# Kernel tuning notes

Measured on AMD Instinct MI355X. Metric: run time of the kernel, lower is better.

The kernel has to match this reference:

```python
import jax, jax.numpy as jnp
import numpy as np

E = 8        # n_experts
TOP_K = 2    # n_activated_experts
B, T, C = 4, 2048, 2048   # batch, seq, d_model
F = 5632     # expert FFN hidden (SwiGLU)


def setup_inputs() -> dict:
    key = jax.random.key(0)
    k = jax.random.split(key, 5)
    s = 0.02  # init scale keeps activations sane
    return {
        "x":  jax.random.normal(k[0], (B, T, C), jnp.float32),
        "Wg": jax.random.normal(k[1], (C, E), jnp.float32) * s,   # gate Linear (no bias)
        "W1": jax.random.normal(k[2], (E, C, F), jnp.float32) * s, # expert gate proj
        "W3": jax.random.normal(k[3], (E, C, F), jnp.float32) * s, # expert up proj
        "W2": jax.random.normal(k[4], (E, F, C), jnp.float32) * s, # expert down proj
    }


def _moe(x, Wg, W1, W3, W2, top_k=TOP_K, norm_probs=True):
    Bb, Tt, Cc = x.shape
    xf = x.reshape(-1, Cc)                                   # [N, C]
    logits = xf @ Wg                                         # [N, E]
    probs = jax.nn.softmax(logits.astype(jnp.float32), axis=-1)
    probs, indices = jax.lax.top_k(probs, top_k)             # [N, K]
    if norm_probs:
        probs = probs / probs.sum(axis=-1, keepdims=True)
    probs = probs.astype(x.dtype)
    N, Ee = xf.shape[0], W1.shape[0]
    # per-token combine weights: w[n, e] = prob if expert e selected for token n else 0
    # (top_k indices are distinct per token, so at most one add per (n, e))
    w = jnp.zeros((N, Ee), x.dtype).at[jnp.arange(N)[:, None], indices].add(probs)
    # scan over experts: weight-0 tokens contribute nothing, matching the sparse
    # masked dispatch/scatter-add of the original exactly.
    def body(y, ws):
        w1, w3, w2, we = ws                                   # we: [N]
        h = jax.nn.silu(xf @ w1) * (xf @ w3)                  # [N, F]
        return y + we[:, None] * (h @ w2), None
    y, _ = jax.lax.scan(body, jnp.zeros_like(xf), (W1, W3, W2, w.T))
    return y.reshape(Bb, Tt, Cc)


def reference(x, Wg, W1, W3, W2):
    return _moe(x, Wg, W1, W3, W2)
```

## Files before the change

### kernel.cpp

```cpp
#include <hip/hip_runtime.h>

#define N_TOK 8192
#define C_DIM 2048
#define F_DIM 5632
#define E_NUM 8
#define BK 64

#define BM 256
#define MAXT 72
#define BN1 128
#define GRID1 (MAXT * (F_DIM/BN1))
#define BN2 256
#define GRID2 (MAXT * (C_DIM/BN2))
#define NT1 (C_DIM/BK)
#define NT2 (F_DIM/BK)

typedef __attribute__((ext_vector_type(8))) short bf16x8;
typedef __attribute__((ext_vector_type(4))) float f32x4;

typedef const void __attribute__((address_space(1)))* gas1;
typedef void __attribute__((address_space(3)))* las3;

__device__ __forceinline__ unsigned short f2bf(float f){
  union { float f; unsigned u; } v; v.f = f;
  unsigned r = v.u + 0x7FFFu + ((v.u >> 16) & 1u);
  return (unsigned short)(r >> 16);
}

__device__ __forceinline__ void glds16(const unsigned short* g, unsigned short* l){
  __builtin_amdgcn_global_load_lds((gas1)g, (las3)l, 16, 0, 0);
}

#define MFMA_BF16 __builtin_amdgcn_mfma_f32_16x16x32_bf16

__global__ void k_cvt_x(const float* __restrict__ x, unsigned short* __restrict__ xb, int n4){
  int i = blockIdx.x * blockDim.x + threadIdx.x;
  int stride = gridDim.x * blockDim.x;
  const float4* xi = (const float4*)x;
  ushort4* xo = (ushort4*)xb;
  for (; i < n4; i += stride){
    float4 v = xi[i];
    ushort4 o; o.x = f2bf(v.x); o.y = f2bf(v.y); o.z = f2bf(v.z); o.w = f2bf(v.w);
    xo[i] = o;
  }
}

__global__ void k_tcvt_w(const float* __restrict__ in, unsigned short* __restrict__ out, int R, int Cc){
  __shared__ float t[64][65];
  size_t slab = (size_t)blockIdx.z * R * Cc;
  in += slab; out += slab;
  int c0 = blockIdx.x * 64, r0 = blockIdx.y * 64;
  int tx = threadIdx.x, ty = threadIdx.y;
  #pragma unroll
  for (int i = 0; i < 16; ++i){
    int r = ty + i*4;
    t[r][tx] = in[(size_t)(r0 + r) * Cc + c0 + tx];
  }
  __syncthreads();
  #pragma unroll
  for (int i = 0; i < 16; ++i){
    int cr = ty + i*4;
    out[(size_t)(c0 + cr) * R + r0 + tx] = f2bf(t[tx][cr]);
  }
}

__global__ void k_router(const float* __restrict__ x, const float* __restrict__ Wg,
                         int* __restrict__ cnt, int* __restrict__ list, float* __restrict__ p_slot)
{
  int wid = threadIdx.x >> 6, lane = threadIdx.x & 63;
  int n = blockIdx.x * 4 + wid;
  int e = lane >> 3, sub = lane & 7;
  const float* xr = x + (size_t)n * C_DIM;
  float acc = 0.f;
  for (int i0 = sub*4; i0 < C_DIM; i0 += 32){
    float4 v = *(const float4*)&xr[i0];
    acc += v.x * Wg[(i0  )*E_NUM + e];
    acc += v.y * Wg[(i0+1)*E_NUM + e];
    acc += v.z * Wg[(i0+2)*E_NUM + e];
    acc += v.w * Wg[(i0+3)*E_NUM + e];
  }
  acc += __shfl_xor(acc, 1);
  acc += __shfl_xor(acc, 2);
  acc += __shfl_xor(acc, 4);
  float lg[E_NUM];
  #pragma unroll
  for (int j = 0; j < E_NUM; ++j) lg[j] = __shfl(acc, j*8);
  if (lane == 0){
    int e1 = 0; float m1 = lg[0];
    #pragma unroll
    for (int j = 1; j < E_NUM; ++j) if (lg[j] > m1){ m1 = lg[j]; e1 = j; }
    int e2 = -1; float m2 = -1e30f;
    #pragma unroll
    for (int j = 0; j < E_NUM; ++j) if (j != e1 && lg[j] > m2){ m2 = lg[j]; e2 = j; }
    float p1 = 1.f / (1.f + __expf(m2 - m1));
    float p2 = 1.f - p1;
    int pos1 = atomicAdd(&cnt[e1], 1);
    list[e1*N_TOK + pos1] = n*2;
    p_slot[n*2] = p1;
    int pos2 = atomicAdd(&cnt[e2], 1);
    list[e2*N_TOK + pos2] = n*2 + 1;
    p_slot[n*2 + 1] = p2;
  }
}

__global__ void k_prefix(const int* __restrict__ cnt, int* __restrict__ meta){
  if (threadIdx.x == 0 && blockIdx.x == 0){
    int acc = 0, t = 0;
    for (int e = 0; e < E_NUM; ++e){
      meta[e] = acc; acc += cnt[e];
      int nt = (cnt[e] + BM - 1) / BM;
      for (int i = 0; i < nt; ++i) meta[16 + t++] = (e << 16) | i;
    }
    meta[8] = t;
  }
}

#define PHASE_ENTER() do{ __builtin_amdgcn_sched_barrier(0); __builtin_amdgcn_s_barrier(); \
                          __builtin_amdgcn_s_setprio(1); } while(0)
#define PHASE_EXIT()  do{ __builtin_amdgcn_s_setprio(0); __builtin_amdgcn_sched_barrier(0); \
                          __builtin_amdgcn_s_barrier(); } while(0)

__global__ __launch_bounds__(512, 2) void k_gemm1(
    const unsigned short* __restrict__ xb,
    const unsigned short* __restrict__ wb1,
    const unsigned short* __restrict__ wb3,
    unsigned short* __restrict__ h,
    const int* __restrict__ cnt,
    const int* __restrict__ meta,
    const int* __restrict__ list)
{
  int o = blockIdx.x;
  int w = (o & 7) * (GRID1/8) + (o >> 3);
  int t = w % MAXT;
  int n0 = (w / MAXT) * BN1;
  if (t >= meta[8]) return;
  int info = meta[16 + t];
  int e  = info >> 16;
  int m0 = (info & 0xffff) * BM;
  int count = cnt[e];
  int hbase = meta[e];

  __shared__ __align__(16) unsigned short lds[2*32768];

  int tid = threadIdx.x;
  int lane = tid & 63, wid = tid >> 6;
  int wm = wid >> 1, wn = wid & 1;
  int l15 = lane & 15;
  int xc0 = (lane >> 4) ^ (lane & 7);
  int xc1 = xc0 ^ 4;

  int srow = tid >> 3;
  int swz = ((tid & 7) ^ (srow & 7)) * 8;
  const unsigned short* aP[4];
  #pragma unroll
  for (int u = 0; u < 4; ++u){
    int ts = list[e*N_TOK + m0 + u*64 + srow];
    int tok = (ts >> 1) & (N_TOK - 1);
    aP[u] = xb + (size_t)tok * C_DIM + swz;
  }
  const unsigned short* bP[4];
  #pragma unroll
  for (int u = 0; u < 4; ++u){
    const unsigned short* base = (u < 2) ? wb1 : wb3;
    bP[u] = base + ((size_t)e*F_DIM + n0 + (u & 1)*64 + srow) * C_DIM + swz;
  }
  int ldw = wid * 512;

  #define ST_A(u, kt) glds16(aP[u] + (kt)*BK, &lds[((kt)&1)*32768 + (u)*4096 + ldw])
  #define ST_B(u, kt) glds16(bP[u] + (kt)*BK, &lds[((kt)&1)*32768 + 16384 + (u)*4096 + ldw])

  ST_A(0,0); ST_A(1,0); ST_A(2,0); ST_A(3,0);
  ST_B(0,0); ST_B(1,0); ST_B(2,0); ST_B(3,0);
  ST_A(0,1); ST_A(1,1); ST_A(2,1); ST_A(3,1);
  asm volatile("s_waitcnt vmcnt(4)" ::: "memory");
  __builtin_amdgcn_sched_barrier(0);
  __builtin_amdgcn_s_barrier();

  f32x4 zero = {0.f, 0.f, 0.f, 0.f};
  f32x4 acc1[4][4], acc3[4][4];
  #pragma unroll
  for (int m = 0; m < 4; ++m)
    #pragma unroll
    for (int q = 0; q < 4; ++q){ acc1[m][q] = zero; acc3[m][q] = zero; }

  for (int kt = 0; kt < NT1; ++kt){
    const unsigned short* bufc = &lds[(kt & 1)*32768];
    bf16x8 a[4][2], b1f[2], b3f[2];
    #pragma unroll
    for (int m = 0; m < 4; ++m){
      int row = wm*64 + m*16 + l15;
      a[m][0] = *(const bf16x8*)&bufc[row*64 + xc0*8];
      a[m][1] = *(const bf16x8*)&bufc[row*64 + xc1*8];
    }
    {
      int brow = wn*64 + l15;
      b1f[0] = *(const bf16x8*)&bufc[16384 + brow*64 + xc0*8];
      b1f[1] = *(const bf16x8*)&bufc[16384 + brow*64 + xc1*8];
      b3f[0] = *(const bf16x8*)&bufc[24576 + brow*64 + xc0*8];
      b3f[1] = *(const bf16x8*)&bufc[24576 + brow*64 + xc1*8];
    }
    ST_B(0, kt+1); ST_B(1, kt+1); ST_B(2, kt+1); ST_B(3, kt+1);
    PHASE_ENTER();
    #pragma unroll
    for (int m = 0; m < 4; ++m){
      acc1[m][0] = MFMA_BF16(a[m][0], b1f[0], acc1[m][0], 0, 0, 0);
      acc1[m][0] = MFMA_BF16(a[m][1], b1f[1], acc1[m][0], 0, 0, 0);
      acc3[m][0] = MFMA_BF16(a[m][0], b3f[0], acc3[m][0], 0, 0, 0);
      acc3[m][0] = MFMA_BF16(a[m][1], b3f[1], acc3[m][0], 0, 0, 0);
    }
    PHASE_EXIT();
    #pragma unroll
    for (int q = 1; q < 4; ++q){
      int brow = wn*64 + q*16 + l15;
      b1f[0] = *(const bf16x8*)&bufc[16384 + brow*64 + xc0*8];
      b1f[1] = *(const bf16x8*)&bufc[16384 + brow*64 + xc1*8];
      b3f[0] = *(const bf16x8*)&bufc[24576 + brow*64 + xc0*8];
      b3f[1] = *(const bf16x8*)&bufc[24576 + brow*64 + xc1*8];
      if (q == 1){ ST_A(0, kt+2); ST_A(1, kt+2); }
      if (q == 2){ ST_A(2, kt+2); ST_A(3, kt+2); }
      PHASE_ENTER();
      #pragma unroll
      for (int m = 0; m < 4; ++m){
        acc1[m][q] = MFMA_BF16(a[m][0], b1f[0], acc1[m][q], 0, 0, 0);
        acc1[m][q] = MFMA_BF16(a[m][1], b1f[1], acc1[m][q], 0, 0, 0);
        acc3[m][q] = MFMA_BF16(a[m][0], b3f[0], acc3[m][q], 0, 0, 0);
        acc3[m][q] = MFMA_BF16(a[m][1], b3f[1], acc3[m][q], 0, 0, 0);
      }
      __builtin_amdgcn_s_setprio(0);
      if (q == 3) asm volatile("s_waitcnt vmcnt(4)" ::: "memory");
      __builtin_amdgcn_sched_barrier(0);
      __builtin_amdgcn_s_barrier();
    }
  }
  asm volatile("s_waitcnt vmcnt(0)" ::: "memory");

  #pragma unroll
  for (int m = 0; m < 4; ++m){
    #pragma unroll
    for (int r = 0; r < 4; ++r){
      int rloc = m0 + wm*64 + m*16 + ((lane >> 4) * 4) + r;
      if (rloc < count){
        unsigned short* hrow = h + (size_t)(hbase + rloc) * F_DIM + n0 + wn*64 + l15;
        #pragma unroll
        for (int q = 0; q < 4; ++q){
          float v1 = acc1[m][q][r];
          float v3 = acc3[m][q][r];
          float hv = (v1 / (1.f + __expf(-v1))) * v3;
          hrow[q*16] = f2bf(hv);
        }
      }
    }
  }
  #undef ST_A
  #undef ST_B
}

__global__ __launch_bounds__(512, 2) void k_gemm2(
    const unsigned short* __restrict__ h,
    const unsigned short* __restrict__ wb2,
    float* __restrict__ y,
    const int* __restrict__ cnt,
    const int* __restrict__ meta,
    const int* __restrict__ list,
    const float* __restrict__ p_slot)
{
  int o = blockIdx.x;
  int w = (o & 7) * (GRID2/8) + (o >> 3);
  int t = w % MAXT;
  int n0 = (w / MAXT) * BN2;
  if (t >= meta[8]) return;
  int info = meta[16 + t];
  int e  = info >> 16;
  int m0 = (info & 0xffff) * BM;
  int count = cnt[e];
  int hbase = meta[e];

  __shared__ __align__(16) unsigned short lds[2*32768];

  int tid = threadIdx.x;
  int lane = tid & 63, wid = tid >> 6;
  int wm = wid >> 1, wn = wid & 1;
  int l15 = lane & 15;
  int xc0 = (lane >> 4) ^ (lane & 7);
  int xc1 = xc0 ^ 4;

  int srow = tid >> 3;
  int swz = ((tid & 7) ^ (srow & 7)) * 8;
  const unsigned short* aP[4];
  #pragma unroll
  for (int u = 0; u < 4; ++u)
    aP[u] = h + (size_t)(hbase + m0 + u*64 + srow) * F_DIM + swz;
  const unsigned short* bP[4];
  #pragma unroll
  for (int u = 0; u < 4; ++u)
    bP[u] = wb2 + ((size_t)e*C_DIM + n0 + u*64 + srow) * F_DIM + swz;
  int ldw = wid * 512;

  #define ST_A2(u, kt) glds16(aP[u] + (kt)*BK, &lds[((kt)&1)*32768 + (u)*4096 + ldw])
  #define ST_B2(u, kt) glds16(bP[u] + (kt)*BK, &lds[((kt)&1)*32768 + 16384 + (u)*4096 + ldw])

  ST_A2(0,0); ST_A2(1,0); ST_A2(2,0); ST_A2(3,0);
  ST_B2(0,0); ST_B2(1,0); ST_B2(2,0); ST_B2(3,0);
  asm volatile("s_waitcnt vmcnt(4)" ::: "memory");
  ST_A2(0,1); ST_A2(1,1); ST_A2(2,1); ST_A2(3,1);
  ST_B2(0,1); ST_B2(2,1);
  asm volatile("s_waitcnt vmcnt(6)" ::: "memory");
  __builtin_amdgcn_sched_barrier(0);
  __builtin_amdgcn_s_barrier();

  f32x4 zero = {0.f, 0.f, 0.f, 0.f};
  f32x4 acc[4][8];
  #pragma unroll
  for (int m = 0; m < 4; ++m)
    #pragma unroll
    for (int nf = 0; nf < 8; ++nf) acc[m][nf] = zero;

  for (int kt = 0; kt < NT2; ++kt){
    const unsigned short* bufc = &lds[(kt & 1)*32768];
    bf16x8 a[4][2], bf[2][2];
    #pragma unroll
    for (int m = 0; m < 4; ++m){
      int row = wm*64 + m*16 + l15;
      a[m][0] = *(const bf16x8*)&bufc[row*64 + xc0*8];
      a[m][1] = *(const bf16x8*)&bufc[row*64 + xc1*8];
    }
    #pragma unroll
    for (int j = 0; j < 2; ++j){
      int brow = wn*128 + j*16 + l15;
      bf[j][0] = *(const bf16x8*)&bufc[16384 + brow*64 + xc0*8];
      bf[j][1] = *(const bf16x8*)&bufc[16384 + brow*64 + xc1*8];
    }
    ST_B2(1, kt+1); ST_B2(3, kt+1);
    PHASE_ENTER();
    #pragma unroll
    for (int m = 0; m < 4; ++m)
      #pragma unroll
      for (int j = 0; j < 2; ++j){
        acc[m][j] = MFMA_BF16(a[m][0], bf[j][0], acc[m][j], 0, 0, 0);
        acc[m][j] = MFMA_BF16(a[m][1], bf[j][1], acc[m][j], 0, 0, 0);
      }
    PHASE_EXIT();
    #pragma unroll
    for (int q = 1; q < 4; ++q){
      #pragma unroll
      for (int j = 0; j < 2; ++j){
        int brow = wn*128 + (q*2 + j)*16 + l15;
        bf[j][0] = *(const bf16x8*)&bufc[16384 + brow*64 + xc0*8];
        bf[j][1] = *(const bf16x8*)&bufc[16384 + brow*64 + xc1*8];
      }
      if (q == 1){ ST_A2(0, kt+2); ST_A2(1, kt+2); }
      if (q == 2){ ST_A2(2, kt+2); ST_A2(3, kt+2); }
      if (q == 3){ ST_B2(0, kt+2); ST_B2(2, kt+2); }
      PHASE_ENTER();
      #pragma unroll
      for (int m = 0; m < 4; ++m)
        #pragma unroll
        for (int j = 0; j < 2; ++j){
          acc[m][q*2+j] = MFMA_BF16(a[m][0], bf[j][0], acc[m][q*2+j], 0, 0, 0);
          acc[m][q*2+j] = MFMA_BF16(a[m][1], bf[j][1], acc[m][q*2+j], 0, 0, 0);
        }
      __builtin_amdgcn_s_setprio(0);
      if (q == 3) asm volatile("s_waitcnt vmcnt(6)" ::: "memory");
      __builtin_amdgcn_sched_barrier(0);
      __builtin_amdgcn_s_barrier();
    }
  }
  asm volatile("s_waitcnt vmcnt(0)" ::: "memory");

  #pragma unroll
  for (int m = 0; m < 4; ++m){
    #pragma unroll
    for (int r = 0; r < 4; ++r){
      int rloc = m0 + wm*64 + m*16 + ((lane >> 4) * 4) + r;
      if (rloc < count){
        int ts = list[e*N_TOK + rloc];
        float p = p_slot[ts];
        int tok = ts >> 1;
        float* yr = y + (size_t)tok * C_DIM + n0 + wn*128 + l15;
        #pragma unroll
        for (int nf = 0; nf < 8; ++nf)
          atomicAdd(&yr[nf*16], p * acc[m][nf][r]);
      }
    }
  }
  #undef ST_A2
  #undef ST_B2
}

extern "C" void kernel_launch(void* const* d_in, const int* in_sizes, int n_in,
                              void* d_out, int out_size, void* d_ws, size_t ws_size,
                              hipStream_t stream)
{
  const float* x  = (const float*)d_in[0];
  const float* Wg = (const float*)d_in[1];
  const float* W1 = (const float*)d_in[2];
  const float* W3 = (const float*)d_in[3];
  const float* W2 = (const float*)d_in[4];
  float* y = (float*)d_out;
  (void)in_sizes; (void)n_in; (void)out_size; (void)ws_size;

  char* ws = (char*)d_ws;
  size_t o = 0;
  auto alloc = [&](size_t bytes)->char* {
    char* p = ws + o;
    o = (o + bytes + 255) & ~(size_t)255;
    return p;
  };
  int*    cnt    = (int*)  alloc(E_NUM * 4);
  int*    meta   = (int*)  alloc(160 * 4);
  float*  p_slot = (float*)alloc((size_t)2*N_TOK * 4);
  int*    list   = (int*)  alloc((size_t)E_NUM*N_TOK * 4);
  unsigned short* xb  = (unsigned short*)alloc((size_t)N_TOK*C_DIM * 2);
  unsigned short* wb1 = (unsigned short*)alloc((size_t)E_NUM*C_DIM*F_DIM * 2);
  unsigned short* wb3 = (unsigned short*)alloc((size_t)E_NUM*C_DIM*F_DIM * 2);
  unsigned short* wb2 = (unsigned short*)alloc((size_t)E_NUM*C_DIM*F_DIM * 2);
  unsigned short* h   = (unsigned short*)alloc((size_t)(2*N_TOK + 1024)*F_DIM * 2);

  hipMemsetAsync(cnt, 0, E_NUM * 4, stream);
  hipMemsetAsync(y, 0, (size_t)N_TOK * C_DIM * 4, stream);
  k_cvt_x<<<4096, 256, 0, stream>>>(x, xb, (N_TOK*C_DIM)/4);
  k_tcvt_w<<<dim3(F_DIM/64, C_DIM/64, E_NUM), dim3(64,4), 0, stream>>>(W1, wb1, C_DIM, F_DIM);
  k_tcvt_w<<<dim3(F_DIM/64, C_DIM/64, E_NUM), dim3(64,4), 0, stream>>>(W3, wb3, C_DIM, F_DIM);
  k_tcvt_w<<<dim3(C_DIM/64, F_DIM/64, E_NUM), dim3(64,4), 0, stream>>>(W2, wb2, F_DIM, C_DIM);
  k_router<<<N_TOK/4, 256, 0, stream>>>(x, Wg, cnt, list, p_slot);
  k_prefix<<<1, 64, 0, stream>>>(cnt, meta);
  k_gemm1<<<GRID1, 512, 0, stream>>>(xb, wb1, wb3, h, cnt, meta, list);
  k_gemm2<<<GRID2, 512, 0, stream>>>(h, wb2, y, cnt, meta, list, p_slot);
}
```

Measured before the change: 1.829 ms.

## Fuse W2 fp32-to-bf16 transpose conversion into down-projection GEMM loads

Drops the separate transpose-convert kernel for W2. The second GEMM now reads fp32 W2 directly through registers, packs it to bf16 with v_cvt_pk_bf16_f32, and writes it transposed into a swizzled LDS layout. The N tile shrinks from 256 to 128 to make room. This removes a full pass that wrote and re-read the bf16 copy of W2. In exchange each W2 tile is read in fp32 (twice the bytes) and re-read by every token tile, and each block does conversion work plus more atomic-output blocks.

```diff
diff --git a/kernel.cpp b/kernel.cpp
--- a/kernel.cpp
+++ b/kernel.cpp
@@ -10,7 +10,7 @@
 #define MAXT 72
 #define BN1 128
 #define GRID1 (MAXT * (F_DIM/BN1))
-#define BN2 256
+#define BN2 128
 #define GRID2 (MAXT * (C_DIM/BN2))
 #define NT1 (C_DIM/BK)
 #define NT2 (F_DIM/BK)
@@ -27,11 +27,18 @@
   return (unsigned short)(r >> 16);
 }
 
+__device__ __forceinline__ unsigned pkbf(float a, float b){
+  unsigned r;
+  asm("v_cvt_pk_bf16_f32 %0, %1, %2" : "=v"(r) : "v"(a), "v"(b));
+  return r;
+}
+
 __device__ __forceinline__ void glds16(const unsigned short* g, unsigned short* l){
   __builtin_amdgcn_global_load_lds((gas1)g, (las3)l, 16, 0, 0);
 }
 
 #define MFMA_BF16 __builtin_amdgcn_mfma_f32_16x16x32_bf16
+#define HSW(v) ((((v) >> 1) ^ ((v) >> 2)) & 7)
 
 __global__ void k_cvt_x(const float* __restrict__ x, unsigned short* __restrict__ xb, int n4){
   int i = blockIdx.x * blockDim.x + threadIdx.x;
@@ -257,7 +264,7 @@
 
 __global__ __launch_bounds__(512, 2) void k_gemm2(
     const unsigned short* __restrict__ h,
-    const unsigned short* __restrict__ wb2,
+    const float* __restrict__ W2,
     float* __restrict__ y,
     const int* __restrict__ cnt,
     const int* __restrict__ meta,
@@ -275,14 +282,14 @@
   int count = cnt[e];
   int hbase = meta[e];
 
-  __shared__ __align__(16) unsigned short lds[2*32768];
+  __shared__ __align__(16) unsigned short lds[2*24576];
 
   int tid = threadIdx.x;
   int lane = tid & 63, wid = tid >> 6;
   int wm = wid >> 1, wn = wid & 1;
   int l15 = lane & 15;
-  int xc0 = (lane >> 4) ^ (lane & 7);
-  int xc1 = xc0 ^ 4;
+  int xcA0 = (lane >> 4) ^ (lane & 7);
+  int xcA1 = xcA0 ^ 4;
 
   int srow = tid >> 3;
   int swz = ((tid & 7) ^ (srow & 7)) * 8;
@@ -290,47 +297,67 @@
   #pragma unroll
   for (int u = 0; u < 4; ++u)
     aP[u] = h + (size_t)(hbase + m0 + u*64 + srow) * F_DIM + swz;
-  const unsigned short* bP[4];
-  #pragma unroll
-  for (int u = 0; u < 4; ++u)
-    bP[u] = wb2 + ((size_t)e*C_DIM + n0 + u*64 + srow) * F_DIM + swz;
   int ldw = wid * 512;
-
-  #define ST_A2(u, kt) glds16(aP[u] + (kt)*BK, &lds[((kt)&1)*32768 + (u)*4096 + ldw])
-  #define ST_B2(u, kt) glds16(bP[u] + (kt)*BK, &lds[((kt)&1)*32768 + 16384 + (u)*4096 + ldw])
-
-  ST_A2(0,0); ST_A2(1,0); ST_A2(2,0); ST_A2(3,0);
-  ST_B2(0,0); ST_B2(1,0); ST_B2(2,0); ST_B2(3,0);
-  asm volatile("s_waitcnt vmcnt(4)" ::: "memory");
-  ST_A2(0,1); ST_A2(1,1); ST_A2(2,1); ST_A2(3,1);
-  ST_B2(0,1); ST_B2(2,1);
-  asm volatile("s_waitcnt vmcnt(6)" ::: "memory");
+  #define ST_A2(u, kt2) glds16(aP[u] + (kt2)*BK, &lds[((kt2)&1)*24576 + (u)*4096 + ldw])
+
+  int fT = (tid >> 5) * 4;
+  int cT = (tid & 31) * 4;
+  const float* wG = W2 + ((size_t)e * F_DIM + fT) * C_DIM + n0 + cT;
+  int fb7 = fT & 7, fb3 = fT >> 3;
+
+  #define LOADW(V, kk) do{ _Pragma("unroll") for (int r_ = 0; r_ < 4; ++r_) \
+      V[r_] = *(const float4*)(wG + (size_t)((kk)*64 + r_) * C_DIM); }while(0)
+  #define CVTW(V, pb) do{ unsigned short* bb_ = &lds[(pb)*24576 + 16384]; \
+      _Pragma("unroll") for (int i_ = 0; i_ < 4; ++i_){ \
+        int c_ = cT + i_; uint2 u_; \
+        u_.x = pkbf(((const float*)&V[0])[i_], ((const float*)&V[1])[i_]); \
+        u_.y = pkbf(((const float*)&V[2])[i_], ((const float*)&V[3])[i_]); \
+        *(uint2*)&bb_[c_*64 + ((fb3 ^ HSW(c_))*8) + fb7] = u_; } }while(0)
+
+  int bch[4], brow[4];
+  #pragma unroll
+  for (int q = 0; q < 4; ++q){
+    int cr = wn*64 + q*16 + l15;
+    bch[q] = HSW(cr); brow[q] = cr*64;
+  }
+
+  f32x4 zero = {0.f, 0.f, 0.f, 0.f};
+  f32x4 acc[4][4];
+  #pragma unroll
+  for (int m = 0; m < 4; ++m)
+    #pragma unroll
+    for (int q = 0; q < 4; ++q) acc[m][q] = zero;
+
+  float4 wv[4], wx[4];
+  LOADW(wv, 0);
+  #pragma unroll
+  for (int u = 0; u < 4; ++u) ST_A2(u, 0);
+  #pragma unroll
+  for (int u = 0; u < 4; ++u) ST_A2(u, 1);
+  CVTW(wv, 0);
+  LOADW(wv, 1);
+  asm volatile("s_waitcnt vmcnt(8)" ::: "memory");
+  asm volatile("s_waitcnt lgkmcnt(0)" ::: "memory");
   __builtin_amdgcn_sched_barrier(0);
   __builtin_amdgcn_s_barrier();
 
-  f32x4 zero = {0.f, 0.f, 0.f, 0.f};
-  f32x4 acc[4][8];
-  #pragma unroll
-  for (int m = 0; m < 4; ++m)
-    #pragma unroll
-    for (int nf = 0; nf < 8; ++nf) acc[m][nf] = zero;
-
   for (int kt = 0; kt < NT2; ++kt){
-    const unsigned short* bufc = &lds[(kt & 1)*32768];
+    const unsigned short* bufc = &lds[(kt & 1)*24576];
+    int k2 = (kt + 2 < NT2) ? kt + 2 : NT2 - 1;
     bf16x8 a[4][2], bf[2][2];
+    LOADW(wx, k2);
     #pragma unroll
     for (int m = 0; m < 4; ++m){
       int row = wm*64 + m*16 + l15;
-      a[m][0] = *(const bf16x8*)&bufc[row*64 + xc0*8];
-      a[m][1] = *(const bf16x8*)&bufc[row*64 + xc1*8];
+      a[m][0] = *(const bf16x8*)&bufc[row*64 + xcA0*8];
+      a[m][1] = *(const bf16x8*)&bufc[row*64 + xcA1*8];
     }
     #pragma unroll
     for (int j = 0; j < 2; ++j){
-      int brow = wn*128 + j*16 + l15;
-      bf[j][0] = *(const bf16x8*)&bufc[16384 + brow*64 + xc0*8];
-      bf[j][1] = *(const bf16x8*)&bufc[16384 + brow*64 + xc1*8];
-    }
-    ST_B2(1, kt+1); ST_B2(3, kt+1);
+      bf[j][0] = *(const bf16x8*)&bufc[16384 + brow[j] + (((lane>>4)    ) ^ bch[j])*8];
+      bf[j][1] = *(const bf16x8*)&bufc[16384 + brow[j] + (((lane>>4) + 4) ^ bch[j])*8];
+    }
+    CVTW(wv, (kt+1)&1);
     PHASE_ENTER();
     #pragma unroll
     for (int m = 0; m < 4; ++m)
@@ -341,29 +368,27 @@
       }
     PHASE_EXIT();
     #pragma unroll
-    for (int q = 1; q < 4; ++q){
+    for (int u = 0; u < 4; ++u) ST_A2(u, kt+2);
+    #pragma unroll
+    for (int j = 0; j < 2; ++j){
+      bf[j][0] = *(const bf16x8*)&bufc[16384 + brow[2+j] + (((lane>>4)    ) ^ bch[2+j])*8];
+      bf[j][1] = *(const bf16x8*)&bufc[16384 + brow[2+j] + (((lane>>4) + 4) ^ bch[2+j])*8];
+    }
+    asm volatile("s_waitcnt vmcnt(8)" ::: "memory");
+    PHASE_ENTER();
+    #pragma unroll
+    for (int m = 0; m < 4; ++m)
       #pragma unroll
       for (int j = 0; j < 2; ++j){
-        int brow = wn*128 + (q*2 + j)*16 + l15;
-        bf[j][0] = *(const bf16x8*)&bufc[16384 + brow*64 + xc0*8];
-        bf[j][1] = *(const bf16x8*)&bufc[16384 + brow*64 + xc1*8];
+        acc[m][2+j] = MFMA_BF16(a[m][0], bf[j][0], acc[m][2+j], 0, 0, 0);
+        acc[m][2+j] = MFMA_BF16(a[m][1], bf[j][1], acc[m][2+j], 0, 0, 0);
       }
-      if (q == 1){ ST_A2(0, kt+2); ST_A2(1, kt+2); }
-      if (q == 2){ ST_A2(2, kt+2); ST_A2(3, kt+2); }
-      if (q == 3){ ST_B2(0, kt+2); ST_B2(2, kt+2); }
-      PHASE_ENTER();
-      #pragma unroll
-      for (int m = 0; m < 4; ++m)
-        #pragma unroll
-        for (int j = 0; j < 2; ++j){
-          acc[m][q*2+j] = MFMA_BF16(a[m][0], bf[j][0], acc[m][q*2+j], 0, 0, 0);
-          acc[m][q*2+j] = MFMA_BF16(a[m][1], bf[j][1], acc[m][q*2+j], 0, 0, 0);
-        }
-      __builtin_amdgcn_s_setprio(0);
-      if (q == 3) asm volatile("s_waitcnt vmcnt(6)" ::: "memory");
-      __builtin_amdgcn_sched_barrier(0);
-      __builtin_amdgcn_s_barrier();
-    }
+    __builtin_amdgcn_s_setprio(0);
+    asm volatile("s_waitcnt lgkmcnt(0)" ::: "memory");
+    __builtin_amdgcn_sched_barrier(0);
+    __builtin_amdgcn_s_barrier();
+    #pragma unroll
+    for (int r = 0; r < 4; ++r) wv[r] = wx[r];
   }
   asm volatile("s_waitcnt vmcnt(0)" ::: "memory");
 
@@ -376,15 +401,16 @@
         int ts = list[e*N_TOK + rloc];
         float p = p_slot[ts];
         int tok = ts >> 1;
-        float* yr = y + (size_t)tok * C_DIM + n0 + wn*128 + l15;
+        float* yr = y + (size_t)tok * C_DIM + n0 + wn*64 + l15;
         #pragma unroll
-        for (int nf = 0; nf < 8; ++nf)
-          atomicAdd(&yr[nf*16], p * acc[m][nf][r]);
+        for (int q = 0; q < 4; ++q)
+          atomicAdd(&yr[q*16], p * acc[m][q][r]);
       }
     }
   }
   #undef ST_A2
-  #undef ST_B2
+  #undef LOADW
+  #undef CVTW
 }
 
 extern "C" void kernel_launch(void* const* d_in, const int* in_sizes, int n_in,
@@ -413,7 +439,6 @@
   unsigned short* xb  = (unsigned short*)alloc((size_t)N_TOK*C_DIM * 2);
   unsigned short* wb1 = (unsigned short*)alloc((size_t)E_NUM*C_DIM*F_DIM * 2);
   unsigned short* wb3 = (unsigned short*)alloc((size_t)E_NUM*C_DIM*F_DIM * 2);
-  unsigned short* wb2 = (unsigned short*)alloc((size_t)E_NUM*C_DIM*F_DIM * 2);
   unsigned short* h   = (unsigned short*)alloc((size_t)(2*N_TOK + 1024)*F_DIM * 2);
 
   hipMemsetAsync(cnt, 0, E_NUM * 4, stream);
@@ -421,9 +446,8 @@
   k_cvt_x<<<4096, 256, 0, stream>>>(x, xb, (N_TOK*C_DIM)/4);
   k_tcvt_w<<<dim3(F_DIM/64, C_DIM/64, E_NUM), dim3(64,4), 0, stream>>>(W1, wb1, C_DIM, F_DIM);
   k_tcvt_w<<<dim3(F_DIM/64, C_DIM/64, E_NUM), dim3(64,4), 0, stream>>>(W3, wb3, C_DIM, F_DIM);
-  k_tcvt_w<<<dim3(C_DIM/64, F_DIM/64, E_NUM), dim3(64,4), 0, stream>>>(W2, wb2, F_DIM, C_DIM);
   k_router<<<N_TOK/4, 256, 0, stream>>>(x, Wg, cnt, list, p_slot);
   k_prefix<<<1, 64, 0, stream>>>(cnt, meta);
   k_gemm1<<<GRID1, 512, 0, stream>>>(xb, wb1, wb3, h, cnt, meta, list);
-  k_gemm2<<<GRID2, 512, 0, stream>>>(h, wb2, y, cnt, meta, list, p_slot);
-}
+  k_gemm2<<<GRID2, 512, 0, stream>>>(h, W2, y, cnt, meta, list, p_slot);
+}
```

New measurement: 2.062 ms. +12.8%, slower.

## Split-K the down-projection GEMM, fuse x conversion into router, merge W1/W3 transposes

Applied to the files above, without the earlier changes.

The down-projection GEMM is split into two K halves, doubling its grid so the work fills the CUs better and the tail is shorter. The halves accumulate into y, which relies on the epilogue adding atomically. The standalone x-to-bf16 kernel is removed and its conversion is folded into the router, which already reads x. The W1 and W3 transpose-convert launches are merged into one launch, which assumes wb3 sits directly after wb1 in the workspace. Together these cut launches and redundant reads, at the cost of extra atomic traffic on y.

```diff
diff --git a/kernel.cpp b/kernel.cpp
--- a/kernel.cpp
+++ b/kernel.cpp
@@ -11,9 +11,11 @@
 #define BN1 128
 #define GRID1 (MAXT * (F_DIM/BN1))
 #define BN2 256
-#define GRID2 (MAXT * (C_DIM/BN2))
+#define KSPLIT 2
+#define GRID2 (MAXT * (C_DIM/BN2) * KSPLIT)
 #define NT1 (C_DIM/BK)
-#define NT2 (F_DIM/BK)
+#define NT2H (F_DIM/BK/KSPLIT)
+#define KHALF (F_DIM/KSPLIT)
 
 typedef __attribute__((ext_vector_type(8))) short bf16x8;
 typedef __attribute__((ext_vector_type(4))) float f32x4;
@@ -33,22 +35,12 @@
 
 #define MFMA_BF16 __builtin_amdgcn_mfma_f32_16x16x32_bf16
 
-__global__ void k_cvt_x(const float* __restrict__ x, unsigned short* __restrict__ xb, int n4){
-  int i = blockIdx.x * blockDim.x + threadIdx.x;
-  int stride = gridDim.x * blockDim.x;
-  const float4* xi = (const float4*)x;
-  ushort4* xo = (ushort4*)xb;
-  for (; i < n4; i += stride){
-    float4 v = xi[i];
-    ushort4 o; o.x = f2bf(v.x); o.y = f2bf(v.y); o.z = f2bf(v.z); o.w = f2bf(v.w);
-    xo[i] = o;
-  }
-}
-
-__global__ void k_tcvt_w(const float* __restrict__ in, unsigned short* __restrict__ out, int R, int Cc){
+__global__ void k_tcvt_w(const float* __restrict__ inA, const float* __restrict__ inB,
+                         unsigned short* __restrict__ out, int R, int Cc){
   __shared__ float t[64][65];
-  size_t slab = (size_t)blockIdx.z * R * Cc;
-  in += slab; out += slab;
+  int z = blockIdx.z;
+  const float* in = (z < 8 ? inA : inB) + (size_t)(z & 7) * R * Cc;
+  out += (size_t)z * R * Cc;
   int c0 = blockIdx.x * 64, r0 = blockIdx.y * 64;
   int tx = threadIdx.x, ty = threadIdx.y;
   #pragma unroll
@@ -65,7 +57,8 @@
 }
 
 __global__ void k_router(const float* __restrict__ x, const float* __restrict__ Wg,
-                         int* __restrict__ cnt, int* __restrict__ list, float* __restrict__ p_slot)
+                         int* __restrict__ cnt, int* __restrict__ list, float* __restrict__ p_slot,
+                         unsigned short* __restrict__ xb)
 {
   int wid = threadIdx.x >> 6, lane = threadIdx.x & 63;
   int n = blockIdx.x * 4 + wid;
@@ -85,6 +78,13 @@
   float lg[E_NUM];
   #pragma unroll
   for (int j = 0; j < E_NUM; ++j) lg[j] = __shfl(acc, j*8);
+  unsigned short* xbr = xb + (size_t)n * C_DIM;
+  #pragma unroll
+  for (int i0 = lane*4; i0 < C_DIM; i0 += 256){
+    float4 v = *(const float4*)&xr[i0];
+    ushort4 u; u.x = f2bf(v.x); u.y = f2bf(v.y); u.z = f2bf(v.z); u.w = f2bf(v.w);
+    *(ushort4*)&xbr[i0] = u;
+  }
   if (lane == 0){
     int e1 = 0; float m1 = lg[0];
     #pragma unroll
@@ -266,8 +266,10 @@
 {
   int o = blockIdx.x;
   int w = (o & 7) * (GRID2/8) + (o >> 3);
-  int t = w % MAXT;
-  int n0 = (w / MAXT) * BN2;
+  int ks = w / (GRID2/KSPLIT);
+  int r2 = w % (GRID2/KSPLIT);
+  int t = r2 % MAXT;
+  int n0 = (r2 / MAXT) * BN2;
   if (t >= meta[8]) return;
   int info = meta[16 + t];
   int e  = info >> 16;
@@ -286,14 +288,15 @@
 
   int srow = tid >> 3;
   int swz = ((tid & 7) ^ (srow & 7)) * 8;
+  size_t kb0 = (size_t)ks * KHALF;
   const unsigned short* aP[4];
   #pragma unroll
   for (int u = 0; u < 4; ++u)
-    aP[u] = h + (size_t)(hbase + m0 + u*64 + srow) * F_DIM + swz;
+    aP[u] = h + (size_t)(hbase + m0 + u*64 + srow) * F_DIM + kb0 + swz;
   const unsigned short* bP[4];
   #pragma unroll
   for (int u = 0; u < 4; ++u)
-    bP[u] = wb2 + ((size_t)e*C_DIM + n0 + u*64 + srow) * F_DIM + swz;
+    bP[u] = wb2 + ((size_t)e*C_DIM + n0 + u*64 + srow) * F_DIM + kb0 + swz;
   int ldw = wid * 512;
 
   #define ST_A2(u, kt) glds16(aP[u] + (kt)*BK, &lds[((kt)&1)*32768 + (u)*4096 + ldw])
@@ -315,7 +318,7 @@
     #pragma unroll
     for (int nf = 0; nf < 8; ++nf) acc[m][nf] = zero;
 
-  for (int kt = 0; kt < NT2; ++kt){
+  for (int kt = 0; kt < NT2H; ++kt){
     const unsigned short* bufc = &lds[(kt & 1)*32768];
     bf16x8 a[4][2], bf[2][2];
     #pragma unroll
@@ -415,15 +418,14 @@
   unsigned short* wb3 = (unsigned short*)alloc((size_t)E_NUM*C_DIM*F_DIM * 2);
   unsigned short* wb2 = (unsigned short*)alloc((size_t)E_NUM*C_DIM*F_DIM * 2);
   unsigned short* h   = (unsigned short*)alloc((size_t)(2*N_TOK + 1024)*F_DIM * 2);
+  (void)wb3;
 
   hipMemsetAsync(cnt, 0, E_NUM * 4, stream);
   hipMemsetAsync(y, 0, (size_t)N_TOK * C_DIM * 4, stream);
-  k_cvt_x<<<4096, 256, 0, stream>>>(x, xb, (N_TOK*C_DIM)/4);
-  k_tcvt_w<<<dim3(F_DIM/64, C_DIM/64, E_NUM), dim3(64,4), 0, stream>>>(W1, wb1, C_DIM, F_DIM);
-  k_tcvt_w<<<dim3(F_DIM/64, C_DIM/64, E_NUM), dim3(64,4), 0, stream>>>(W3, wb3, C_DIM, F_DIM);
-  k_tcvt_w<<<dim3(C_DIM/64, F_DIM/64, E_NUM), dim3(64,4), 0, stream>>>(W2, wb2, F_DIM, C_DIM);
-  k_router<<<N_TOK/4, 256, 0, stream>>>(x, Wg, cnt, list, p_slot);
+  k_router<<<N_TOK/4, 256, 0, stream>>>(x, Wg, cnt, list, p_slot, xb);
   k_prefix<<<1, 64, 0, stream>>>(cnt, meta);
+  k_tcvt_w<<<dim3(F_DIM/64, C_DIM/64, 2*E_NUM), dim3(64,4), 0, stream>>>(W1, W3, wb1, C_DIM, F_DIM);
+  k_tcvt_w<<<dim3(C_DIM/64, F_DIM/64, E_NUM), dim3(64,4), 0, stream>>>(W2, W2, wb2, F_DIM, C_DIM);
   k_gemm1<<<GRID1, 512, 0, stream>>>(xb, wb1, wb3, h, cnt, meta, list);
   k_gemm2<<<GRID2, 512, 0, stream>>>(h, wb2, y, cnt, meta, list, p_slot);
 }
```

Measured after the change: 1.834 ms. No clear change (+0.3%).
